# Performance work log

Measured on AMD Instinct MI355X. Metric: run time of the kernel, lower is better.

The kernel has to match this reference:

```python
import jax, jax.numpy as jnp
import numpy as np
from math import sqrt

HEADS = 16
DIM_HEAD = 64
EPS = 1e-4
MP_T = 0.3


def l2norm(t, eps=EPS):
    n = jnp.linalg.norm(t, axis=-1, keepdims=True)
    return t / jnp.maximum(n, eps)


def mp_linear(x, w):
    # weight-normalized linear: l2norm rows / sqrt(fan_in)
    fan_in = w.shape[1]
    wn = l2norm(w) / sqrt(fan_in)
    return x @ wn.T


def setup_inputs() -> dict:
    key = jax.random.key(0)
    k1, k2, k3, k4 = jax.random.split(key, 4)
    b, n, dim = 2, 2048, 1024
    x = jax.random.normal(k1, (b, n, dim), dtype=jnp.float32)
    w_qkv = jax.random.normal(k2, (3 * HEADS * DIM_HEAD, dim), dtype=jnp.float32)
    w_out = jax.random.normal(k3, (dim, HEADS * DIM_HEAD), dtype=jnp.float32)
    mem_kv = jax.random.normal(k4, (2, HEADS, 4, DIM_HEAD), dtype=jnp.float32)
    return {"x": x, "w_qkv": w_qkv, "w_out": w_out, "mem_kv": mem_kv}


def reference(x, w_qkv, w_out, mem_kv):
    b, n, dim = x.shape
    h, d = HEADS, DIM_HEAD
    scale = d ** -0.5

    qkv = mp_linear(x, w_qkv)                      # [b, n, 3*h*d]
    q, k, v = jnp.split(qkv, 3, axis=-1)
    split_heads = lambda t: t.reshape(b, n, h, d).transpose(0, 2, 1, 3)  # b h n d
    q, k, v = map(split_heads, (q, k, v))

    mk = jnp.broadcast_to(mem_kv[0], (b, h, mem_kv.shape[2], d))
    mv = jnp.broadcast_to(mem_kv[1], (b, h, mem_kv.shape[2], d))
    k = jnp.concatenate([mk, k], axis=2)
    v = jnp.concatenate([mv, v], axis=2)

    # pixel_norm: l2 normalize over head dim, rescale by sqrt(d)
    pn = lambda t: l2norm(t) * sqrt(d)
    q, k, v = pn(q), pn(k), pn(v)

    q = q * scale
    sim = jnp.einsum('bhid,bhjd->bhij', q, k)
    attn = jax.nn.softmax(sim, axis=-1)
    out = jnp.einsum('bhij,bhjd->bhid', attn, v)
    out = out.transpose(0, 2, 1, 3).reshape(b, n, h * d)
    out = mp_linear(out, w_out)

    # magnitude-preserving residual add
    t = MP_T
    return (out * (1.0 - t) + x * t) / sqrt((1.0 - t) ** 2 + t ** 2)
```

## Files before the change

kernel.cpp:

```cpp
#include <hip/hip_runtime.h>
#include <hip/hip_bf16.h>
#include <math.h>


#define EPSN 1e-4f
#define NKEY 2112
#define LOG2E 1.4426950408889634f

typedef __attribute__((ext_vector_type(8))) short short8;
typedef __attribute__((ext_vector_type(4))) short short4v;
typedef __attribute__((ext_vector_type(4))) float floatx4;

typedef __attribute__((address_space(1))) const void g_void;
typedef __attribute__((address_space(3))) void lds_void;

__device__ __forceinline__ void async16(void* lds, const void* g) {
    __builtin_amdgcn_global_load_lds((g_void*)g, (lds_void*)lds, 16, 0, 0);
}

__device__ __forceinline__ short f2bf(float f) {
    union { float f; unsigned u; } c{f};
    unsigned r = (c.u + 0x7FFF + ((c.u >> 16) & 1)) >> 16;
    return (short)r;
}
__device__ __forceinline__ short f2bf_fast(float f) {
    union { float f; unsigned u; } c{f};
    return (short)((c.u + 0x8000) >> 16);
}

__global__ __launch_bounds__(256) void prep_inputs(const float* __restrict__ x,
                                                   const float* __restrict__ w_qkv,
                                                   const float* __restrict__ w_out,
                                                   const float* __restrict__ memkv,
                                                   short* __restrict__ xb,
                                                   short* __restrict__ wnqkv,
                                                   short* __restrict__ wnout,
                                                   short* __restrict__ Kb,
                                                   short* __restrict__ Vt) {
    const int bid = blockIdx.x, tid = threadIdx.x;
    if (bid < 4096) {
        int i = bid * 1024 + tid * 4;
        float4 v = *(const float4*)(x + i);
        short4v s = {f2bf(v.x), f2bf(v.y), f2bf(v.z), f2bf(v.w)};
        *(short4v*)(xb + i) = s;
        return;
    }
    if (bid < 8192) {
        const float* w; short* wn; int r;
        if (bid < 7168) { w = w_qkv; wn = wnqkv; r = bid - 4096; }
        else            { w = w_out; wn = wnout; r = bid - 7168; }
        __shared__ float red[256];
        const float* row = w + (size_t)r * 1024;
        float ss = 0.f;
        for (int c = tid; c < 1024; c += 256) { float v = row[c]; ss += v * v; }
        red[tid] = ss;
        __syncthreads();
        for (int s = 128; s > 0; s >>= 1) {
            if (tid < s) red[tid] += red[tid + s];
            __syncthreads();
        }
        float f = 1.0f / (fmaxf(sqrtf(red[0]), EPSN) * 32.0f);
        for (int c = tid; c < 1024; c += 256) wn[(size_t)r * 1024 + c] = f2bf(row[c] * f);
        return;
    }
    const int bh = bid - 8192, h = bh & 15;
    const int r = tid >> 2, part = tid & 3;
    if (r < 4) {
        const float* pk = memkv + (size_t)(h * 4 + r) * 64 + part * 16;
        const float* pv = memkv + (size_t)((16 + h) * 4 + r) * 64 + part * 16;
        float k[16], v[16]; float ssk = 0.f, ssv = 0.f;
        #pragma unroll
        for (int i = 0; i < 16; i += 4) {
            float4 a = *(const float4*)(pk + i);
            float4 b = *(const float4*)(pv + i);
            k[i]=a.x; k[i+1]=a.y; k[i+2]=a.z; k[i+3]=a.w;
            v[i]=b.x; v[i+1]=b.y; v[i+2]=b.z; v[i+3]=b.w;
            ssk += a.x*a.x + a.y*a.y + a.z*a.z + a.w*a.w;
            ssv += b.x*b.x + b.y*b.y + b.z*b.z + b.w*b.w;
        }
        ssk += __shfl_xor(ssk, 1); ssk += __shfl_xor(ssk, 2);
        ssv += __shfl_xor(ssv, 1); ssv += __shfl_xor(ssv, 2);
        const float fk = 8.0f / fmaxf(sqrtf(ssk), EPSN);
        const float fv = 8.0f / fmaxf(sqrtf(ssv), EPSN);
        short* kd = Kb + ((size_t)bh * NKEY + r) * 64 + part * 16;
        #pragma unroll
        for (int i = 0; i < 16; i++) kd[i] = f2bf(k[i] * fk);
        #pragma unroll
        for (int i = 0; i < 16; i++)
            Vt[((size_t)bh * 64 + part * 16 + i) * NKEY + r] = f2bf(v[i] * fv);
    }
    for (int p = tid; p < 480; p += 256)
        *(short8*)(Kb + ((size_t)bh * NKEY + 2052) * 64 + p * 8) = (short8){0,0,0,0,0,0,0,0};
    for (int p = tid; p < 960; p += 256) {
        int row = p / 15, c = p % 15;
        *(short4v*)(Vt + ((size_t)bh * 64 + row) * NKEY + 2052 + c * 4) = (short4v){0,0,0,0};
    }
}

__global__ __launch_bounds__(256) void gemm_qkv(const short* __restrict__ A,
                                                const short* __restrict__ B,
                                                short* __restrict__ Qb,
                                                short* __restrict__ Kb,
                                                short* __restrict__ Vt) {
    constexpr int K = 1024;
    __shared__ __align__(16) short As[2][128 * 32];
    __shared__ __align__(16) short Bs[2][128 * 32];
    const int tid = threadIdx.x;
    const int wv = tid >> 6, lane = tid & 63;
    const int l16 = lane & 15, quad = lane >> 4;
    const int wr = wv >> 1, wc = wv & 1;
    const int bm0 = blockIdx.y * 128, bn0 = blockIdx.x * 128;
    const int grow = lane >> 2;
    const int gk = (lane & 3) * 8;

    floatx4 acc[4][4];
    #pragma unroll
    for (int i = 0; i < 4; i++)
        #pragma unroll
        for (int j = 0; j < 4; j++) acc[i][j] = (floatx4){0.f, 0.f, 0.f, 0.f};

    const short* Abase = A + (size_t)(bm0 + wv * 32 + grow) * K + gk;
    const short* Bbase = B + (size_t)(bn0 + wv * 32 + grow) * K + gk;

    #pragma unroll
    for (int j = 0; j < 2; j++) {
        async16(&As[0][(wv * 32 + j * 16) * 32], Abase + (size_t)(j * 16) * K);
        async16(&Bs[0][(wv * 32 + j * 16) * 32], Bbase + (size_t)(j * 16) * K);
    }
    const int NKI = K >> 5;
    for (int ki = 0; ki < NKI; ki++) {
        const int cur = ki & 1;
        if (ki + 1 < NKI) {
            const int nxt = cur ^ 1;
            const int off = (ki + 1) * 32;
            #pragma unroll
            for (int j = 0; j < 2; j++) {
                async16(&As[nxt][(wv * 32 + j * 16) * 32], Abase + (size_t)(j * 16) * K + off);
                async16(&Bs[nxt][(wv * 32 + j * 16) * 32], Bbase + (size_t)(j * 16) * K + off);
            }
            asm volatile("s_waitcnt vmcnt(4)" ::: "memory");
        } else {
            asm volatile("s_waitcnt vmcnt(0)" ::: "memory");
        }
        asm volatile("s_barrier" ::: "memory");
        short8 aA[4], bB[4];
        #pragma unroll
        for (int i = 0; i < 4; i++)
            aA[i] = *(const short8*)&As[cur][(wr * 64 + i * 16 + l16) * 32 + quad * 8];
        #pragma unroll
        for (int j = 0; j < 4; j++)
            bB[j] = *(const short8*)&Bs[cur][(wc * 64 + j * 16 + l16) * 32 + quad * 8];
        #pragma unroll
        for (int i = 0; i < 4; i++)
            #pragma unroll
            for (int j = 0; j < 4; j++)
                acc[i][j] = __builtin_amdgcn_mfma_f32_16x16x32_bf16(aA[i], bB[j], acc[i][j], 0, 0, 0);
        asm volatile("s_barrier" ::: "memory");
    }

    const int colbase = bn0 + wc * 64;
    const int which = colbase >> 10;
    const int h = (colbase >> 6) & 15;
    float sc[4][4];
    #pragma unroll
    for (int i = 0; i < 4; i++)
        #pragma unroll
        for (int r = 0; r < 4; r++) {
            float ss = 0.f;
            #pragma unroll
            for (int j = 0; j < 4; j++) ss += acc[i][j][r] * acc[i][j][r];
            ss += __shfl_xor(ss, 1); ss += __shfl_xor(ss, 2);
            ss += __shfl_xor(ss, 4); ss += __shfl_xor(ss, 8);
            const float num = (which == 0) ? LOG2E : 8.0f;
            sc[i][r] = num / fmaxf(sqrtf(ss), EPSN);
        }
    if (which == 2) {
        #pragma unroll
        for (int i = 0; i < 4; i++) {
            const int row0 = bm0 + wr * 64 + i * 16 + quad * 4;
            const int bh = (row0 >> 11) * 16 + h;
            const int tok0 = row0 & 2047;
            #pragma unroll
            for (int j = 0; j < 4; j++) {
                const int d = j * 16 + l16;
                short4v o = {f2bf(acc[i][j][0] * sc[i][0]), f2bf(acc[i][j][1] * sc[i][1]),
                             f2bf(acc[i][j][2] * sc[i][2]), f2bf(acc[i][j][3] * sc[i][3])};
                *(short4v*)(Vt + ((size_t)bh * 64 + d) * NKEY + 4 + tok0) = o;
            }
        }
    } else {
        #pragma unroll
        for (int i = 0; i < 4; i++)
            #pragma unroll
            for (int r = 0; r < 4; r++) {
                const int row = bm0 + wr * 64 + i * 16 + quad * 4 + r;
                const int bh = (row >> 11) * 16 + h;
                const int tok = row & 2047;
                const size_t base = (which == 0) ? ((size_t)bh * 2048 + tok) * 64
                                                 : ((size_t)bh * NKEY + 4 + tok) * 64;
                short* dst = (which == 0) ? Qb : Kb;
                #pragma unroll
                for (int j = 0; j < 4; j++)
                    dst[base + j * 16 + l16] = f2bf(acc[i][j][r] * sc[i][r]);
            }
    }
}

template<int MT, int NT>
__global__ __launch_bounds__(256) void gemm_mfma(const short* __restrict__ A,
                                                 const short* __restrict__ B,
                                                 float* __restrict__ C,
                                                 int M, int N, int K,
                                                 const float* __restrict__ resid) {
    constexpr int FI = MT / 32;
    constexpr int FJ = NT / 32;
    constexpr int nA = MT / 64;
    constexpr int nB = NT / 64;
    __shared__ __align__(16) short As[2][MT * 32];
    __shared__ __align__(16) short Bs[2][NT * 32];
    const int tid = threadIdx.x;
    const int wv = tid >> 6, lane = tid & 63;
    const int l16 = lane & 15, quad = lane >> 4;
    const int wr = wv >> 1, wc = wv & 1;
    const int bm0 = blockIdx.y * MT, bn0 = blockIdx.x * NT;
    const int grow = lane >> 2;
    const int gk = (lane & 3) * 8;

    floatx4 acc[FI][FJ];
    #pragma unroll
    for (int i = 0; i < FI; i++)
        #pragma unroll
        for (int j = 0; j < FJ; j++) acc[i][j] = (floatx4){0.f, 0.f, 0.f, 0.f};

    const short* Abase = A + (size_t)(bm0 + wv * (MT / 4) + grow) * K + gk;
    const short* Bbase = B + (size_t)(bn0 + wv * (NT / 4) + grow) * K + gk;

    #pragma unroll
    for (int j = 0; j < nA; j++)
        async16(&As[0][(wv * (MT / 4) + j * 16) * 32], Abase + (size_t)(j * 16) * K);
    #pragma unroll
    for (int j = 0; j < nB; j++)
        async16(&Bs[0][(wv * (NT / 4) + j * 16) * 32], Bbase + (size_t)(j * 16) * K);

    const int NKI = K >> 5;
    for (int ki = 0; ki < NKI; ki++) {
        const int cur = ki & 1;
        if (ki + 1 < NKI) {
            const int nxt = cur ^ 1;
            const int off = (ki + 1) * 32;
            #pragma unroll
            for (int j = 0; j < nA; j++)
                async16(&As[nxt][(wv * (MT / 4) + j * 16) * 32], Abase + (size_t)(j * 16) * K + off);
            #pragma unroll
            for (int j = 0; j < nB; j++)
                async16(&Bs[nxt][(wv * (NT / 4) + j * 16) * 32], Bbase + (size_t)(j * 16) * K + off);
            if constexpr (nA + nB == 4)      asm volatile("s_waitcnt vmcnt(4)" ::: "memory");
            else if constexpr (nA + nB == 3) asm volatile("s_waitcnt vmcnt(3)" ::: "memory");
            else                             asm volatile("s_waitcnt vmcnt(2)" ::: "memory");
        } else {
            asm volatile("s_waitcnt vmcnt(0)" ::: "memory");
        }
        asm volatile("s_barrier" ::: "memory");
        short8 aA[FI], bB[FJ];
        #pragma unroll
        for (int i = 0; i < FI; i++)
            aA[i] = *(const short8*)&As[cur][(wr * (MT / 2) + i * 16 + l16) * 32 + quad * 8];
        #pragma unroll
        for (int j = 0; j < FJ; j++)
            bB[j] = *(const short8*)&Bs[cur][(wc * (NT / 2) + j * 16 + l16) * 32 + quad * 8];
        #pragma unroll
        for (int i = 0; i < FI; i++)
            #pragma unroll
            for (int j = 0; j < FJ; j++)
                acc[i][j] = __builtin_amdgcn_mfma_f32_16x16x32_bf16(aA[i], bB[j], acc[i][j], 0, 0, 0);
        asm volatile("s_barrier" ::: "memory");
    }
    #pragma unroll
    for (int i = 0; i < FI; i++)
        #pragma unroll
        for (int j = 0; j < FJ; j++)
            #pragma unroll
            for (int r = 0; r < 4; r++) {
                const int row = bm0 + wr * (MT / 2) + i * 16 + quad * 4 + r;
                const int col = bn0 + wc * (NT / 2) + j * 16 + l16;
                const size_t idx = (size_t)row * N + col;
                float v = acc[i][j][r];
                if (resid) v = (v * 0.7f + resid[idx] * 0.3f) * 1.3130643285972254f;
                C[idx] = v;
            }
}

__global__ __launch_bounds__(64) void attn_mfma(const short* __restrict__ Qb,
                                                const short* __restrict__ Kb,
                                                const short* __restrict__ Vt,
                                                short* __restrict__ attnb) {
    const int bh = blockIdx.x;
    const int q0 = blockIdx.y * 64;
    const int lane = threadIdx.x;
    const int l16 = lane & 15, quad = lane >> 4;

    __shared__ __align__(16) short Pw[64 * 72];

    const short* qbase = Qb + ((size_t)bh * 2048 + q0 + l16) * 64;
    short8 bQ[4][2];
    #pragma unroll
    for (int qg = 0; qg < 4; qg++)
        #pragma unroll
        for (int dh = 0; dh < 2; dh++)
            bQ[qg][dh] = *(const short8*)(qbase + qg * 16 * 64 + dh * 32 + quad * 8);

    floatx4 O[4][4];
    #pragma unroll
    for (int dt = 0; dt < 4; dt++)
        #pragma unroll
        for (int qg = 0; qg < 4; qg++) O[dt][qg] = (floatx4){0.f, 0.f, 0.f, 0.f};
    float lp[4] = {0.f, 0.f, 0.f, 0.f};

    const short* kb = Kb + (size_t)bh * NKEY * 64;
    const short* vb = Vt + (size_t)bh * 64 * NKEY;

    for (int tile = 0; tile < 33; tile++) {
        short8 aK[4][2], aV[4][2];
        #pragma unroll
        for (int kt = 0; kt < 4; kt++)
            #pragma unroll
            for (int dh = 0; dh < 2; dh++)
                aK[kt][dh] = *(const short8*)(kb + ((size_t)(tile * 64 + kt * 16 + l16)) * 64 + dh * 32 + quad * 8);
        #pragma unroll
        for (int dt = 0; dt < 4; dt++)
            #pragma unroll
            for (int kh = 0; kh < 2; kh++)
                aV[dt][kh] = *(const short8*)(vb + ((size_t)(dt * 16 + l16)) * NKEY + tile * 64 + kh * 32 + quad * 8);

        #pragma unroll
        for (int kt = 0; kt < 4; kt++) {
            #pragma unroll
            for (int qg = 0; qg < 4; qg++) {
                floatx4 s = (floatx4){-12.f, -12.f, -12.f, -12.f};
                s = __builtin_amdgcn_mfma_f32_16x16x32_bf16(aK[kt][0], bQ[qg][0], s, 0, 0, 0);
                s = __builtin_amdgcn_mfma_f32_16x16x32_bf16(aK[kt][1], bQ[qg][1], s, 0, 0, 0);
                if (tile == 32 && (kt > 0 || quad > 0))
                    s = (floatx4){-1e30f, -1e30f, -1e30f, -1e30f};
                float p0 = __builtin_amdgcn_exp2f(s[0]);
                float p1 = __builtin_amdgcn_exp2f(s[1]);
                float p2 = __builtin_amdgcn_exp2f(s[2]);
                float p3 = __builtin_amdgcn_exp2f(s[3]);
                lp[qg] += (p0 + p1) + (p2 + p3);
                short4v pk = {f2bf_fast(p0), f2bf_fast(p1), f2bf_fast(p2), f2bf_fast(p3)};
                *(short4v*)&Pw[(qg * 16 + l16) * 72 + kt * 16 + quad * 4] = pk;
            }
        }
        short8 bP[4][2];
        #pragma unroll
        for (int qg = 0; qg < 4; qg++)
            #pragma unroll
            for (int kh = 0; kh < 2; kh++)
                bP[qg][kh] = *(const short8*)&Pw[(qg * 16 + l16) * 72 + kh * 32 + quad * 8];
        #pragma unroll
        for (int dt = 0; dt < 4; dt++)
            #pragma unroll
            for (int qg = 0; qg < 4; qg++) {
                O[dt][qg] = __builtin_amdgcn_mfma_f32_16x16x32_bf16(aV[dt][0], bP[qg][0], O[dt][qg], 0, 0, 0);
                O[dt][qg] = __builtin_amdgcn_mfma_f32_16x16x32_bf16(aV[dt][1], bP[qg][1], O[dt][qg], 0, 0, 0);
            }
    }

    const int bb = bh >> 4, h = bh & 15;
    #pragma unroll
    for (int qg = 0; qg < 4; qg++) {
        float l = lp[qg];
        l += __shfl_xor(l, 16);
        l += __shfl_xor(l, 32);
        const float inv = 1.0f / l;
        const int token = q0 + qg * 16 + l16;
        #pragma unroll
        for (int dt = 0; dt < 4; dt++) {
            short4v o = {f2bf(O[dt][qg][0] * inv), f2bf(O[dt][qg][1] * inv),
                         f2bf(O[dt][qg][2] * inv), f2bf(O[dt][qg][3] * inv)};
            *(short4v*)(attnb + ((size_t)(bb * 2048 + token)) * 1024 + h * 64 + dt * 16 + quad * 4) = o;
        }
    }
}

extern "C" void kernel_launch(void* const* d_in, const int* in_sizes, int n_in,
                              void* d_out, int out_size, void* d_ws, size_t ws_size,
                              hipStream_t stream) {
    const float* x      = (const float*)d_in[0];
    const float* w_qkv  = (const float*)d_in[1];
    const float* w_out  = (const float*)d_in[2];
    const float* mem_kv = (const float*)d_in[3];
    float* out = (float*)d_out;

    char* ws = (char*)d_ws;
    short* wnqkv_b = (short*)(ws);
    short* wnout_b = (short*)(ws + (6u << 20));
    short* xb      = (short*)(ws + (8u << 20));
    short* Qb      = (short*)(ws + (16u << 20));
    short* Kb      = (short*)(ws + (24u << 20));
    short* Vt      = (short*)(ws + (33u << 20));
    short* attnb   = (short*)(ws + (42u << 20));

    prep_inputs<<<8224, 256, 0, stream>>>(x, w_qkv, w_out, mem_kv,
                                          xb, wnqkv_b, wnout_b, Kb, Vt);

    gemm_qkv<<<dim3(3072 / 128, 4096 / 128), 256, 0, stream>>>(
        xb, wnqkv_b, Qb, Kb, Vt);

    attn_mfma<<<dim3(32, 32), 64, 0, stream>>>(Qb, Kb, Vt, attnb);

    gemm_mfma<128, 64><<<dim3(1024 / 64, 4096 / 128), 256, 0, stream>>>(
        attnb, wnout_b, out, 4096, 1024, 1024, x);
}
```

Baseline: 229.2 us.

## Split attention key tiles across four waves with LDS reduction

The attention kernel grows from one wave to four waves per block. Each wave processes every fourth key tile for the same 64 queries, and the partial outputs and row sums are combined through shared memory before normalizing and writing bf16. The aim is more parallelism and better latency hiding per query tile, since each block previously ran a single wave over all 33 tiles. In exchange it adds LDS traffic, syncthreads barriers, more shared memory per block, and redundant Q loads in every wave. It relies on the fixed softmax offset (no running max), which makes the partial sums directly addable.

```diff
diff --git a/kernel.cpp b/kernel.cpp
--- a/kernel.cpp
+++ b/kernel.cpp
@@ -290,16 +290,21 @@
             }
 }
 
-__global__ __launch_bounds__(64) void attn_mfma(const short* __restrict__ Qb,
-                                                const short* __restrict__ Kb,
-                                                const short* __restrict__ Vt,
-                                                short* __restrict__ attnb) {
+__global__ __launch_bounds__(256, 3) void attn_mfma(const short* __restrict__ Qb,
+                                                    const short* __restrict__ Kb,
+                                                    const short* __restrict__ Vt,
+                                                    short* __restrict__ attnb) {
     const int bh = blockIdx.x;
     const int q0 = blockIdx.y * 64;
-    const int lane = threadIdx.x;
+    const int tid = threadIdx.x;
+    const int wave = tid >> 6, lane = tid & 63;
     const int l16 = lane & 15, quad = lane >> 4;
 
-    __shared__ __align__(16) short Pw[64 * 72];
+    __shared__ __align__(16) char lbuf[36864 + 1024];
+    short* Pw   = (short*)lbuf + wave * 4608;
+    float* Ared = (float*)lbuf;
+    float* Bred = (float*)(lbuf + 17408);
+    float* lpW  = (float*)(lbuf + 34816);
 
     const short* qbase = Qb + ((size_t)bh * 2048 + q0 + l16) * 64;
     short8 bQ[4][2];
@@ -319,7 +324,7 @@
     const short* kb = Kb + (size_t)bh * NKEY * 64;
     const short* vb = Vt + (size_t)bh * 64 * NKEY;
 
-    for (int tile = 0; tile < 33; tile++) {
+    for (int tile = wave; tile < 33; tile += 4) {
         short8 aK[4][2], aV[4][2];
         #pragma unroll
         for (int kt = 0; kt < 4; kt++)
@@ -365,21 +370,66 @@
             }
     }
 
+    float lpq[4];
+    #pragma unroll
+    for (int qg = 0; qg < 4; qg++) {
+        float v = lp[qg];
+        v += __shfl_xor(v, 16);
+        v += __shfl_xor(v, 32);
+        lpq[qg] = v;
+    }
+
+    __syncthreads();
+    if (quad == 0) {
+        #pragma unroll
+        for (int qg = 0; qg < 4; qg++) lpW[wave * 64 + qg * 16 + l16] = lpq[qg];
+    }
+    if (wave == 2 || wave == 3) {
+        float* R = (wave == 2) ? Ared : Bred;
+        #pragma unroll
+        for (int dt = 0; dt < 4; dt++)
+            #pragma unroll
+            for (int qg = 0; qg < 4; qg++)
+                *(floatx4*)&R[(qg * 16 + l16) * 68 + dt * 16 + quad * 4] = O[dt][qg];
+    }
+    __syncthreads();
+    if (wave == 0 || wave == 1) {
+        float* R = (wave == 0) ? Ared : Bred;
+        #pragma unroll
+        for (int dt = 0; dt < 4; dt++)
+            #pragma unroll
+            for (int qg = 0; qg < 4; qg++) {
+                floatx4 t = *(floatx4*)&R[(qg * 16 + l16) * 68 + dt * 16 + quad * 4];
+                t += O[dt][qg];
+                *(floatx4*)&R[(qg * 16 + l16) * 68 + dt * 16 + quad * 4] = t;
+            }
+    }
+    __syncthreads();
+
     const int bb = bh >> 4, h = bh & 15;
-    #pragma unroll
-    for (int qg = 0; qg < 4; qg++) {
-        float l = lp[qg];
-        l += __shfl_xor(l, 16);
-        l += __shfl_xor(l, 32);
-        const float inv = 1.0f / l;
-        const int token = q0 + qg * 16 + l16;
-        #pragma unroll
-        for (int dt = 0; dt < 4; dt++) {
-            short4v o = {f2bf(O[dt][qg][0] * inv), f2bf(O[dt][qg][1] * inv),
-                         f2bf(O[dt][qg][2] * inv), f2bf(O[dt][qg][3] * inv)};
-            *(short4v*)(attnb + ((size_t)(bb * 2048 + token)) * 1024 + h * 64 + dt * 16 + quad * 4) = o;
-        }
-    }
+    const int q = tid >> 2, dc = (tid & 3) * 16;
+    const int qg2 = q >> 4, ql = q & 15;
+    const float denom = lpW[qg2 * 16 + ql] + lpW[64 + qg2 * 16 + ql] +
+                        lpW[128 + qg2 * 16 + ql] + lpW[192 + qg2 * 16 + ql];
+    const float inv = 1.0f / denom;
+    short8 o0, o1;
+    #pragma unroll
+    for (int i = 0; i < 2; i++) {
+        floatx4 a = *(floatx4*)&Ared[q * 68 + dc + i * 4];
+        floatx4 b = *(floatx4*)&Bred[q * 68 + dc + i * 4];
+        #pragma unroll
+        for (int j = 0; j < 4; j++) o0[i * 4 + j] = f2bf((a[j] + b[j]) * inv);
+    }
+    #pragma unroll
+    for (int i = 0; i < 2; i++) {
+        floatx4 a = *(floatx4*)&Ared[q * 68 + dc + 8 + i * 4];
+        floatx4 b = *(floatx4*)&Bred[q * 68 + dc + 8 + i * 4];
+        #pragma unroll
+        for (int j = 0; j < 4; j++) o1[i * 4 + j] = f2bf((a[j] + b[j]) * inv);
+    }
+    short* dst = attnb + ((size_t)(bb * 2048 + q0 + q)) * 1024 + h * 64 + dc;
+    *(short8*)dst = o0;
+    *(short8*)(dst + 8) = o1;
 }
 
 extern "C" void kernel_launch(void* const* d_in, const int* in_sizes, int n_in,
@@ -406,7 +456,7 @@
     gemm_qkv<<<dim3(3072 / 128, 4096 / 128), 256, 0, stream>>>(
         xb, wnqkv_b, Qb, Kb, Vt);
 
-    attn_mfma<<<dim3(32, 32), 64, 0, stream>>>(Qb, Kb, Vt, attnb);
+    attn_mfma<<<dim3(32, 32), 256, 0, stream>>>(Qb, Kb, Vt, attnb);
 
     gemm_mfma<128, 64><<<dim3(1024 / 64, 4096 / 128), 256, 0, stream>>>(
         attnb, wnout_b, out, 4096, 1024, 1024, x);
```

Result: slower. 479.2 us (+109.1%).
